# Kernel tuning notes

Measured on AMD Instinct MI355X. Metric: run time of the kernel, lower is better.

The kernel has to match this reference:

```python
import jax, jax.numpy as jnp
import numpy as np

SEARCH_RANGE = 4  # matches init_kwargs


def setup_inputs() -> dict:
    key = jax.random.key(0)
    k1, k2 = jax.random.split(key)
    shape = (8, 256, 64, 128)  # [B, C, H, W]
    feature1 = jax.random.normal(k1, shape, dtype=jnp.float32)
    feature2 = jax.random.normal(k2, shape, dtype=jnp.float32)
    return {"feature1": feature1, "feature2": feature2}


def reference(feature1, feature2):
    R = SEARCH_RANGE
    b, c, h, w = feature1.shape
    # zero-pad feature2 spatially by R on each side
    f2p = jnp.pad(feature2, ((0, 0), (0, 0), (R, R), (R, R)))
    D = 2 * R + 1
    # shift offsets in the same order as the original nested loop (idx outer, jdx inner)
    offsets = jnp.stack(
        jnp.meshgrid(jnp.arange(D), jnp.arange(D), indexing="ij"), axis=-1
    ).reshape(-1, 2)  # [81, 2]

    def corr_one(ij):
        win = jax.lax.dynamic_slice(f2p, (0, 0, ij[0], ij[1]), (b, c, h, w))
        return jnp.sum(feature1 * win, axis=1)  # [B, H, W]

    dots = jax.vmap(corr_one)(offsets)  # [81, B, H, W]
    return jnp.transpose(dots, (1, 0, 2, 3))  # [B, 81, H, W]
```

## Files before the change

### kernel.cpp

```cpp
#include <hip/hip_runtime.h>
#include <cstdint>

typedef __attribute__((ext_vector_type(8))) short short8;
typedef __attribute__((ext_vector_type(4))) float floatx4;
typedef __attribute__((ext_vector_type(2))) unsigned int uintx2;
typedef __attribute__((ext_vector_type(4))) unsigned int uintx4;

#define CS 18
#define A_WORDS (8 * 16 * CS)
#define B_ROWS  13
#define B_WORDS (B_ROWS * 24 * CS)

__device__ __forceinline__ uint32_t pack2(float a, float b) {
    uint32_t ua = __builtin_bit_cast(uint32_t, a);
    uint32_t ub = __builtin_bit_cast(uint32_t, b);
    ua = (ua + 0x7FFFu + ((ua >> 16) & 1u)) >> 16;
    ub = (ub + 0x7FFFu + ((ub >> 16) & 1u)) >> 16;
    return ua | (ub << 16);
}

__device__ __forceinline__ short8 frag_ld(const uint32_t* p) {
    uintx2 lo = *(const uintx2*)p;
    uintx2 hi = *(const uintx2*)(p + 2);
    uintx4 v = {lo.x, lo.y, hi.x, hi.y};
    return __builtin_bit_cast(short8, v);
}

__global__ __launch_bounds__(512, 4)
void corr_kernel(const float* __restrict__ f1, const float* __restrict__ f2,
                 float* __restrict__ out) {
    __shared__ uint32_t ldsA[2 * A_WORDS];
    __shared__ uint32_t ldsB[2 * B_WORDS];

    const int tid  = threadIdx.x;
    const int lane = tid & 63;
    const int wh   = tid >> 6;
    const int n15  = lane & 15;
    const int q    = lane >> 4;

    const int bid    = blockIdx.x;
    const int b      = bid & 7;
    const int dihalf = (bid >> 3) & 1;
    const int ht     = (bid >> 4) & 7;
    const int wt     = bid >> 7;

    const int w0 = wt * 16;
    const int h0 = ht * 8;
    const int h  = h0 + wh;

    const int diN    = dihalf ? 4 : 5;
    const int diBase = dihalf * 5;
    const int ghBase = dihalf ? (h0 + 1) : (h0 - 4);

    const float* f1b = f1 + (size_t)b * 256 * 8192;
    const float* f2b = f2 + (size_t)b * 256 * 8192;

    const int aw4 = tid & 3, akp = (tid >> 2) & 15, arow = tid >> 6;
    int aOffG = (2 * akp) * 8192 + (h0 + arow) * 128 + (w0 + 4 * aw4);
    const int aLds = (arow * 16 + 4 * aw4) * CS + akp;

    int bOffG[3];
    int bLds[3];
    uint32_t bMask[3];
#pragma unroll
    for (int s = 0; s < 3; ++s) {
        int t = tid + 512 * s;
        int w4 = t % 6;
        int r2 = t / 6;
        int kp = r2 & 15, row = r2 >> 4;
        int gh = ghBase + row;
        int gw = w0 - 4 + 4 * w4;
        bool live = (t < 1152);
        bool inb  = live && ((unsigned)gh < 64u) && ((unsigned)gw < 128u);
        bOffG[s] = inb ? ((2 * kp) * 8192 + gh * 128 + gw) : 0;
        bLds[s]  = live ? ((row * 24 + 4 * w4) * CS + kp)
                        : ((12 * 24 + (tid & 7)) * CS);
        bMask[s] = inb ? 0xFFFFFFFFu : 0u;
    }

    floatx4 acc[5][2];
#pragma unroll
    for (int dl = 0; dl < 5; ++dl)
#pragma unroll
        for (int t = 0; t < 2; ++t)
            acc[dl][t] = (floatx4){0.f, 0.f, 0.f, 0.f};

    floatx4 rA[2], rB[3][2];
    uint32_t pkA[4], pkB[12];

    auto issue = [&]() {
        rA[0] = *(const floatx4*)(f1b + aOffG);
        rA[1] = *(const floatx4*)(f1b + aOffG + 8192);
        aOffG += 32 * 8192;
#pragma unroll
        for (int s = 0; s < 3; ++s) {
            rB[s][0] = *(const floatx4*)(f2b + bOffG[s]);
            rB[s][1] = *(const floatx4*)(f2b + bOffG[s] + 8192);
            bOffG[s] += 32 * 8192;
        }
    };
    auto packall = [&]() {
#pragma unroll
        for (int i = 0; i < 4; ++i)
            pkA[i] = pack2(rA[0][i], rA[1][i]);
#pragma unroll
        for (int s = 0; s < 3; ++s)
#pragma unroll
            for (int i = 0; i < 4; ++i)
                pkB[4 * s + i] = pack2(rB[s][0][i], rB[s][1][i]) & bMask[s];
    };

    issue();
    packall();

    for (int ch = 0; ch < 8; ++ch) {
        uint32_t* bufA = ldsA + (ch & 1) * A_WORDS;
        uint32_t* bufB = ldsB + (ch & 1) * B_WORDS;

#pragma unroll
        for (int i = 0; i < 4; ++i)
            bufA[aLds + i * CS] = pkA[i];
#pragma unroll
        for (int s = 0; s < 3; ++s)
#pragma unroll
            for (int i = 0; i < 4; ++i)
                bufB[bLds[s] + i * CS] = pkB[4 * s + i];

        if (ch < 7) issue();
        __syncthreads();

        const uint32_t* pa = bufA + (wh * 16 + n15) * CS + 4 * q;
        short8 a0 = frag_ld(pa);
        const uint32_t* pb = bufB + (wh * 24 + n15) * CS + 4 * q;
#pragma unroll
        for (int dl = 0; dl < 5; ++dl) {
            if (dl < diN) {
                const uint32_t* p = pb + dl * (24 * CS);
                short8 b0 = frag_ld(p);
                short8 b1 = frag_ld(p + 8 * CS);
                acc[dl][0] = __builtin_amdgcn_mfma_f32_16x16x32_bf16(a0, b0, acc[dl][0], 0, 0, 0);
                acc[dl][1] = __builtin_amdgcn_mfma_f32_16x16x32_bf16(a0, b1, acc[dl][1], 0, 0, 0);
            }
        }
        if (ch < 7) packall();
    }

    const size_t base = ((size_t)b * 81) * 8192 + (size_t)h * 128 + w0;
#pragma unroll
    for (int dl = 0; dl < 5; ++dl) {
        if (dl < diN) {
            const int dio = diBase + dl;
#pragma unroll
            for (int t = 0; t < 2; ++t) {
#pragma unroll
                for (int r = 0; r < 4; ++r) {
                    int mp = 4 * q + r;
                    int dj = t * 8 + n15 - mp;
                    if (dj >= 0 && dj <= 8 && (t == 0 || n15 >= 8)) {
                        out[base + (size_t)(dio * 9 + dj) * 8192 + mp] = acc[dl][t][r];
                    }
                }
            }
        }
    }
}

extern "C" void kernel_launch(void* const* d_in, const int* in_sizes, int n_in,
                              void* d_out, int out_size, void* d_ws, size_t ws_size,
                              hipStream_t stream) {
    const float* f1 = (const float*)d_in[0];
    const float* f2 = (const float*)d_in[1];
    float* out = (float*)d_out;
    corr_kernel<<<dim3(1024), dim3(512), 0, stream>>>(f1, f2, out);
}
```

Measured before the change: 187.8 us.

## Pre-transpose feature2 to padded bf16 channel-last layout and use direct LDS loads

Adds a pre-pass kernel that converts feature2 to bf16 channel-pair words in a padded [B,H,W+pad,C/2] workspace layout with zeroed borders. The main kernel then streams feature2 tiles into LDS with global_load_lds using an XOR swizzle, and reads feature1 straight from global into registers. Each block now covers all 9 row offsets instead of splitting them across two blocks, which halves the grid and removes redundant feature1 loads and in-kernel packing of feature2. In exchange it costs an extra kernel launch and a full read and write of the transposed feature2, and it depends on the workspace being large enough, falling back to the old kernel otherwise.

```diff
diff --git a/kernel.cpp b/kernel.cpp
--- a/kernel.cpp
+++ b/kernel.cpp
@@ -5,11 +5,6 @@
 typedef __attribute__((ext_vector_type(4))) float floatx4;
 typedef __attribute__((ext_vector_type(2))) unsigned int uintx2;
 typedef __attribute__((ext_vector_type(4))) unsigned int uintx4;
-
-#define CS 18
-#define A_WORDS (8 * 16 * CS)
-#define B_ROWS  13
-#define B_WORDS (B_ROWS * 24 * CS)
 
 __device__ __forceinline__ uint32_t pack2(float a, float b) {
     uint32_t ua = __builtin_bit_cast(uint32_t, a);
@@ -19,6 +14,167 @@
     return ua | (ub << 16);
 }
 
+#define T2P_WORDS ((size_t)8 * 64 * 144 * 128)
+#define WS_NEED   (T2P_WORDS * 4 + 4096)
+
+__global__ __launch_bounds__(256)
+void transpose_f2(const float* __restrict__ f2, uint32_t* __restrict__ t2p) {
+    __shared__ float t[64][33];
+    const int tid = threadIdx.x;
+    const int bid = blockIdx.x;
+    const int b = bid & 7, h = (bid >> 3) & 63, wt = bid >> 9;
+    const int w0 = wt * 32;
+    const float* f2b = f2 + (size_t)b * 256 * 8192 + (size_t)h * 128 + w0;
+    uint32_t* t2row = t2p + ((size_t)(b * 64 + h) * 144 + (w0 + 4)) * 128;
+
+    const int rw = tid & 31, rc8 = tid >> 5;
+    const int kpL = tid & 31, wg = tid >> 5;
+
+    for (int cc = 0; cc < 4; ++cc) {
+        if (cc) __syncthreads();
+#pragma unroll
+        for (int i = 0; i < 8; ++i)
+            t[rc8 * 8 + i][rw] = f2b[(size_t)(cc * 64 + rc8 * 8 + i) * 8192 + rw];
+        __syncthreads();
+#pragma unroll
+        for (int j = 0; j < 4; ++j) {
+            int w = wg * 4 + j;
+            t2row[(size_t)w * 128 + cc * 32 + kpL] = pack2(t[2 * kpL][w], t[2 * kpL + 1][w]);
+        }
+    }
+    if (wt == 0) {
+        uint32_t* p = t2p + ((size_t)(b * 64 + h) * 144) * 128;
+        for (int idx = tid; idx < 512; idx += 256) p[idx] = 0;
+    }
+    if (wt == 3) {
+        uint32_t* p = t2p + ((size_t)(b * 64 + h) * 144 + 132) * 128;
+        for (int idx = tid; idx < 1536; idx += 256) p[idx] = 0;
+    }
+    if (bid == 0) {
+        uint32_t* z = t2p + T2P_WORDS;
+        for (int idx = tid; idx < 1024; idx += 256) z[idx] = 0;
+    }
+}
+
+#define AS1 __attribute__((address_space(1)))
+#define AS3 __attribute__((address_space(3)))
+
+__device__ __forceinline__ void gld_lds16(const uint32_t* src, uint32_t* dst) {
+    __builtin_amdgcn_global_load_lds((const AS1 void*)src, (AS3 void*)dst, 16, 0, 0);
+}
+
+__global__ __launch_bounds__(512, 4)
+void corr2(const float* __restrict__ f1, const uint32_t* __restrict__ t2p,
+           const uint32_t* __restrict__ wsZ, float* __restrict__ out) {
+    __shared__ uint32_t ldsB[2 * 8192];
+
+    const int tid  = threadIdx.x;
+    const int lane = tid & 63;
+    const int wh   = tid >> 6;
+    const int n15  = lane & 15;
+    const int q    = lane >> 4;
+
+    const int bid = blockIdx.x;
+    const int b  = bid & 7;
+    const int ht = (bid >> 3) & 7;
+    const int wt = bid >> 6;
+    const int h0 = 8 * ht, w0 = 16 * wt;
+    const int h  = h0 + wh;
+
+    const float* f1b = f1 + (size_t)b * 256 * 8192;
+
+    const uint32_t* bsrc[4];
+    int bstep[4], bdst[4];
+#pragma unroll
+    for (int ki = 0; ki < 4; ++ki) {
+        int k = 4 * wh + ki, r = k >> 1, gh = h0 - 4 + r;
+        int c = (k & 1) * 16 + (lane >> 2);
+        int gd = (lane & 3) ^ ((c >> 1) & 3);
+        bool ok = (unsigned)gh < 64u;
+        bsrc[ki]  = ok ? t2p + ((size_t)(b * 64 + gh) * 144 + (w0 + c)) * 128 + gd * 4
+                       : wsZ + lane * 4;
+        bstep[ki] = ok ? 16 : 0;
+        bdst[ki]  = k * 256;
+    }
+
+    const float* aP = f1b + (size_t)(8 * q) * 8192 + (size_t)h * 128 + w0 + n15;
+
+    floatx4 acc[9][2];
+#pragma unroll
+    for (int di = 0; di < 9; ++di)
+#pragma unroll
+        for (int t = 0; t < 2; ++t)
+            acc[di][t] = (floatx4){0.f, 0.f, 0.f, 0.f};
+
+#pragma unroll
+    for (int ki = 0; ki < 4; ++ki) { gld_lds16(bsrc[ki], &ldsB[bdst[ki]]); bsrc[ki] += bstep[ki]; }
+    __builtin_amdgcn_sched_barrier(0);
+    float rAn[8];
+#pragma unroll
+    for (int j = 0; j < 8; ++j) rAn[j] = aP[(size_t)j * 8192];
+
+    const int rdB = n15 * 16 + ((q ^ ((n15 >> 1) & 3)) << 2);
+
+    for (int ch = 0; ch < 8; ++ch) {
+        asm volatile("s_waitcnt vmcnt(8)\n\ts_barrier" ::: "memory");
+        const int cb = (ch & 1) * 8192;
+
+        float rAc[8];
+#pragma unroll
+        for (int j = 0; j < 8; ++j) rAc[j] = rAn[j];
+
+        if (ch < 7) {
+            const int nb = ((ch + 1) & 1) * 8192;
+#pragma unroll
+            for (int ki = 0; ki < 4; ++ki) { gld_lds16(bsrc[ki], &ldsB[nb + bdst[ki]]); bsrc[ki] += bstep[ki]; }
+            __builtin_amdgcn_sched_barrier(0);
+            aP += (size_t)32 * 8192;
+#pragma unroll
+            for (int j = 0; j < 8; ++j) rAn[j] = aP[(size_t)j * 8192];
+        }
+
+        uint32_t aw0 = pack2(rAc[0], rAc[1]);
+        uint32_t aw1 = pack2(rAc[2], rAc[3]);
+        uint32_t aw2 = pack2(rAc[4], rAc[5]);
+        uint32_t aw3 = pack2(rAc[6], rAc[7]);
+        uintx4 av = {aw0, aw1, aw2, aw3};
+        short8 a0 = __builtin_bit_cast(short8, av);
+
+        const uint32_t* bufB = ldsB + cb;
+#pragma unroll
+        for (int di = 0; di < 9; ++di) {
+            const uint32_t* p0 = bufB + (wh + di) * 512 + rdB;
+            uintx4 v0 = *(const uintx4*)p0;
+            uintx4 v1 = *(const uintx4*)(p0 + 128);
+            short8 b0 = __builtin_bit_cast(short8, v0);
+            short8 b1 = __builtin_bit_cast(short8, v1);
+            acc[di][0] = __builtin_amdgcn_mfma_f32_16x16x32_bf16(a0, b0, acc[di][0], 0, 0, 0);
+            acc[di][1] = __builtin_amdgcn_mfma_f32_16x16x32_bf16(a0, b1, acc[di][1], 0, 0, 0);
+        }
+    }
+
+    const size_t base = ((size_t)b * 81) * 8192 + (size_t)h * 128 + w0;
+#pragma unroll
+    for (int di = 0; di < 9; ++di) {
+#pragma unroll
+        for (int t = 0; t < 2; ++t) {
+#pragma unroll
+            for (int r = 0; r < 4; ++r) {
+                int mp = 4 * q + r;
+                int dj = t * 8 + n15 - mp;
+                if (dj >= 0 && dj <= 8 && (t == 0 || n15 >= 8)) {
+                    out[base + (size_t)(di * 9 + dj) * 8192 + mp] = acc[di][t][r];
+                }
+            }
+        }
+    }
+}
+
+#define CS 18
+#define A_WORDS (8 * 16 * CS)
+#define B_ROWS  13
+#define B_WORDS (B_ROWS * 24 * CS)
+
 __device__ __forceinline__ short8 frag_ld(const uint32_t* p) {
     uintx2 lo = *(const uintx2*)p;
     uintx2 hi = *(const uintx2*)(p + 2);
@@ -30,7 +186,7 @@
 void corr_kernel(const float* __restrict__ f1, const float* __restrict__ f2,
                  float* __restrict__ out) {
     __shared__ uint32_t ldsA[2 * A_WORDS];
-    __shared__ uint32_t ldsB[2 * B_WORDS];
+    __shared__ uint32_t ldsB2[2 * B_WORDS];
 
     const int tid  = threadIdx.x;
     const int lane = tid & 63;
@@ -59,9 +215,7 @@
     int aOffG = (2 * akp) * 8192 + (h0 + arow) * 128 + (w0 + 4 * aw4);
     const int aLds = (arow * 16 + 4 * aw4) * CS + akp;
 
-    int bOffG[3];
-    int bLds[3];
-    uint32_t bMask[3];
+    int bOffG[3]; int bLds[3]; uint32_t bMask[3];
 #pragma unroll
     for (int s = 0; s < 3; ++s) {
         int t = tid + 512 * s;
@@ -73,8 +227,7 @@
         bool live = (t < 1152);
         bool inb  = live && ((unsigned)gh < 64u) && ((unsigned)gw < 128u);
         bOffG[s] = inb ? ((2 * kp) * 8192 + gh * 128 + gw) : 0;
-        bLds[s]  = live ? ((row * 24 + 4 * w4) * CS + kp)
-                        : ((12 * 24 + (tid & 7)) * CS);
+        bLds[s]  = live ? ((row * 24 + 4 * w4) * CS + kp) : ((12 * 24 + (tid & 7)) * CS);
         bMask[s] = inb ? 0xFFFFFFFFu : 0u;
     }
 
@@ -101,8 +254,7 @@
     };
     auto packall = [&]() {
 #pragma unroll
-        for (int i = 0; i < 4; ++i)
-            pkA[i] = pack2(rA[0][i], rA[1][i]);
+        for (int i = 0; i < 4; ++i) pkA[i] = pack2(rA[0][i], rA[1][i]);
 #pragma unroll
         for (int s = 0; s < 3; ++s)
 #pragma unroll
@@ -110,22 +262,17 @@
                 pkB[4 * s + i] = pack2(rB[s][0][i], rB[s][1][i]) & bMask[s];
     };
 
-    issue();
-    packall();
+    issue(); packall();
 
     for (int ch = 0; ch < 8; ++ch) {
         uint32_t* bufA = ldsA + (ch & 1) * A_WORDS;
-        uint32_t* bufB = ldsB + (ch & 1) * B_WORDS;
-
-#pragma unroll
-        for (int i = 0; i < 4; ++i)
-            bufA[aLds + i * CS] = pkA[i];
+        uint32_t* bufB = ldsB2 + (ch & 1) * B_WORDS;
+#pragma unroll
+        for (int i = 0; i < 4; ++i) bufA[aLds + i * CS] = pkA[i];
 #pragma unroll
         for (int s = 0; s < 3; ++s)
 #pragma unroll
-            for (int i = 0; i < 4; ++i)
-                bufB[bLds[s] + i * CS] = pkB[4 * s + i];
-
+            for (int i = 0; i < 4; ++i) bufB[bLds[s] + i * CS] = pkB[4 * s + i];
         if (ch < 7) issue();
         __syncthreads();
 
@@ -171,5 +318,11 @@
     const float* f1 = (const float*)d_in[0];
     const float* f2 = (const float*)d_in[1];
     float* out = (float*)d_out;
-    corr_kernel<<<dim3(1024), dim3(512), 0, stream>>>(f1, f2, out);
-}
+    if (ws_size >= WS_NEED && d_ws != nullptr) {
+        uint32_t* t2p = (uint32_t*)d_ws;
+        transpose_f2<<<dim3(2048), dim3(256), 0, stream>>>(f2, t2p);
+        corr2<<<dim3(512), dim3(512), 0, stream>>>(f1, t2p, t2p + T2P_WORDS, out);
+    } else {
+        corr_kernel<<<dim3(1024), dim3(512), 0, stream>>>(f1, f2, out);
+    }
+}
```

New measurement: 188.5 us. No clear change (+0.4%).
